# Kernel optimization log

Hardware: AMD Instinct MI355X
Metric: run time of the kernel (lower is better)

Reference implementation:

```python
import math
import jax, jax.numpy as jnp
import numpy as np

B, S, D = 4, 2048, 1024
H, HD = 16, 64
NUM_BUCKETS = 32
MAX_DISTANCE = 128
EPS = 1e-6
ENC_S = 512


def _relative_position_bucket(relative_position):
    # bidirectional=False path
    num_buckets = NUM_BUCKETS
    rp = -jnp.minimum(relative_position, 0)  # [S, S] nonneg
    max_exact = num_buckets // 2
    is_small = rp < max_exact
    scale = (num_buckets - max_exact) / math.log(MAX_DISTANCE / max_exact)
    large = max_exact + (jnp.log(jnp.maximum(rp, 1).astype(jnp.float32) / max_exact) * scale).astype(jnp.int32)
    large = jnp.minimum(large, num_buckets - 1)
    return jnp.where(is_small, rp, large)


def compute_bias(rel_emb, q_len, k_len):
    ctx = jnp.arange(q_len)[:, None]
    mem = jnp.arange(k_len)[None, :]
    bucket = _relative_position_bucket(mem - ctx)          # [q, k] int
    values = rel_emb[bucket]                                # [q, k, H]
    return jnp.transpose(values, (2, 0, 1))[None]           # [1, H, q, k]


def setup_inputs() -> dict:
    key = jax.random.key(0)
    ks = jax.random.split(key, 8)
    std = 0.02
    return {
        "input_ids": jax.random.normal(ks[0], (B, S, D), jnp.float32),
        "encoder_output": jax.random.normal(ks[1], (B, ENC_S, D), jnp.float32),
        "wq": jax.random.normal(ks[2], (D, H * HD), jnp.float32) * std,
        "wk": jax.random.normal(ks[3], (D, H * HD), jnp.float32) * std,
        "wv": jax.random.normal(ks[4], (D, H * HD), jnp.float32) * std,
        "wo": jax.random.normal(ks[5], (H * HD, D), jnp.float32) * std,
        "rel_emb": jax.random.normal(ks[6], (NUM_BUCKETS, H), jnp.float32) * std,
        "ln_w": jnp.ones((D,), jnp.float32),
    }


def reference(input_ids, encoder_output, wq, wk, wv, wo, rel_emb, ln_w):
    origin = input_ids
    # MT5LayerNorm: RMS norm, no mean subtraction, no bias
    variance = jnp.mean(jnp.square(input_ids.astype(jnp.float32)), axis=-1, keepdims=True)
    x = (input_ids * jax.lax.rsqrt(variance + EPS)) * ln_w

    q = (x @ wq).reshape(B, S, H, HD)
    k = (x @ wk).reshape(B, S, H, HD)
    v = (x @ wv).reshape(B, S, H, HD)

    # NOTE: T5-style attention has no 1/sqrt(d) scaling
    scores = jnp.einsum("bqhd,bkhd->bhqk", q, k)
    scores = scores + compute_bias(rel_emb, S, S)
    attn = jax.nn.softmax(scores, axis=-1)
    ctx = jnp.einsum("bhqk,bkhd->bqhd", attn, v).reshape(B, S, H * HD)
    attn_out = ctx @ wo

    # residual connection (dropout is identity at rate 0 / eval)
    return origin + attn_out
```

## Files before the change

### kernel.cpp

```cpp
#include <hip/hip_runtime.h>
#include <hip/hip_bf16.h>
#include <math.h>

#define S_LEN 2048
#define D_DIM 1024
#define NHEAD 16

typedef __attribute__((ext_vector_type(8))) short bf16x8;
typedef __attribute__((ext_vector_type(4))) float floatx4;

__device__ __forceinline__ short f32_bf16(float f) {
  union { float f; unsigned u; } v; v.f = f;
  unsigned r = v.u + 0x7FFFu + ((v.u >> 16) & 1u);
  return (short)(r >> 16);
}

__device__ __forceinline__ float exp2_fast(float x) {
#if __has_builtin(__builtin_amdgcn_exp2f)
  return __builtin_amdgcn_exp2f(x);
#else
  float r; asm("v_exp_f32 %0, %1" : "=v"(r) : "v"(x)); return r;
#endif
}

__device__ __forceinline__ void gload16(const void* g, void* l) {
  __builtin_amdgcn_global_load_lds((const __attribute__((address_space(1))) unsigned*)g,
                                   (__attribute__((address_space(3))) unsigned*)l,
                                   16, 0, 0);
}

__global__ __launch_bounds__(256) void prep_k(const float* __restrict__ x,
                                              const float* __restrict__ lnw,
                                              const float* __restrict__ wq,
                                              const float* __restrict__ wk,
                                              const float* __restrict__ wv,
                                              const float* __restrict__ wo,
                                              short* __restrict__ xb,
                                              short* __restrict__ oqkv,
                                              short* __restrict__ owo) {
  if (blockIdx.x < 8192) {
    int row = blockIdx.x;
    const float4* xr = (const float4*)(x + (size_t)row * D_DIM);
    float4 v = xr[threadIdx.x];
    float ss = v.x*v.x + v.y*v.y + v.z*v.z + v.w*v.w;
    #pragma unroll
    for (int off = 32; off > 0; off >>= 1) ss += __shfl_xor(ss, off);
    __shared__ float red[4];
    if ((threadIdx.x & 63) == 0) red[threadIdx.x >> 6] = ss;
    __syncthreads();
    float scale = rsqrtf((red[0]+red[1]+red[2]+red[3]) * (1.f/D_DIM) + 1e-6f);
    float4 wv4 = ((const float4*)lnw)[threadIdx.x];
    short4 o;
    o.x = f32_bf16(v.x*scale*wv4.x);
    o.y = f32_bf16(v.y*scale*wv4.y);
    o.z = f32_bf16(v.z*scale*wv4.z);
    o.w = f32_bf16(v.w*scale*wv4.w);
    ((short4*)xb)[(size_t)row*256 + threadIdx.x] = o;
  } else {
    __shared__ float tile[64][65];
    int id = blockIdx.x - 8192;
    int m  = id >> 8;
    int tt = id & 255;
    int tn = tt >> 4, tk = tt & 15;
    const float* src = (m == 0) ? wq : (m == 1) ? wk : (m == 2) ? wv : wo;
    float scale = (m == 0) ? 1.44269504f : 1.0f;
    int t = threadIdx.x;
    int kl  = t >> 4;
    int nl4 = t & 15;
    #pragma unroll
    for (int i = 0; i < 4; i++) {
      int k = i*16 + kl;
      float4 v = *(const float4*)&src[(size_t)(tk*64 + k)*1024 + tn*64 + nl4*4];
      tile[k][nl4*4+0] = v.x;
      tile[k][nl4*4+1] = v.y;
      tile[k][nl4*4+2] = v.z;
      tile[k][nl4*4+3] = v.w;
    }
    __syncthreads();
    short* dst = (m < 3) ? oqkv : owo;
    size_t nbase = (m < 3) ? (size_t)m * 1024 : 0;
    #pragma unroll
    for (int i = 0; i < 2; i++) {
      int idx = i*256 + t;
      int nl = idx >> 3;
      int g  = idx & 7;
      short tmp[8];
      #pragma unroll
      for (int j = 0; j < 8; j++) tmp[j] = f32_bf16(tile[g*8 + j][nl] * scale);
      *(bf16x8*)&dst[(nbase + tn*64 + nl)*1024 + tk*64 + g*8] = *(bf16x8*)tmp;
    }
  }
}

template<bool ADD_RES, int PANELS, bool WRITE_VT>
__global__ __launch_bounds__(256) void gemm_bt(const short* __restrict__ A,
                                               const short* __restrict__ Bt,
                                               short* __restrict__ Cb,
                                               float* __restrict__ Cf,
                                               const float* __restrict__ res,
                                               short* __restrict__ vt,
                                               int M, int N, int K) {
  constexpr int BK = 32;
  __shared__ __align__(16) short As[2][128*BK];
  __shared__ __align__(16) short Bs[2][128*BK];
  int tid = threadIdx.x;
  int w = tid >> 6, lane = tid & 63, quad = lane >> 4, l16 = lane & 15;
  int wr = w >> 1, wc = w & 1;
  const int id = blockIdx.x;
  const int xcd = id & 7, g = id >> 3;
  const int bm = g / PANELS;
  const int bn = xcd * PANELS + (g % PANELS);
  const short* Ag = A + (size_t)bm * 128 * K;
  const short* Bg = Bt + (size_t)bn * 128 * K;
  const int r4 = lane >> 2;
  const int c4 = lane & 3;
  const int lc = c4 ^ (r4 & 3);
  const int swz = (quad ^ (l16 & 3)) * 8;

  floatx4 acc[4][4] = {};

  #define GSTAGE(p_, k0_) do {                                                  \
    _Pragma("unroll")                                                           \
    for (int i = 0; i < 2; i++) {                                               \
      int c = w + i*4;                                                          \
      gload16(Ag + (size_t)(c*16 + r4) * K + (k0_) + lc*8, &As[p_][c*16*BK]);   \
      gload16(Bg + (size_t)(c*16 + r4) * K + (k0_) + lc*8, &Bs[p_][c*16*BK]);   \
    }                                                                           \
  } while (0)

  GSTAGE(0, 0);
  int p = 0;
  for (int k0 = 0; k0 < K; k0 += BK) {
    __syncthreads();
    if (k0 + BK < K) GSTAGE(p ^ 1, k0 + BK);
    bf16x8 af[4], bfr[4];
    #pragma unroll
    for (int i = 0; i < 4; i++) {
      af[i]  = *(const bf16x8*)&As[p][(wr*64 + i*16 + l16)*BK + swz];
      bfr[i] = *(const bf16x8*)&Bs[p][(wc*64 + i*16 + l16)*BK + swz];
    }
    #pragma unroll
    for (int i = 0; i < 4; i++)
      #pragma unroll
      for (int j = 0; j < 4; j++)
        acc[i][j] = __builtin_amdgcn_mfma_f32_16x16x32_bf16(af[i], bfr[j], acc[i][j], 0, 0, 0);
    p ^= 1;
  }
  #undef GSTAGE

  if (WRITE_VT && bn >= 16) {
    #pragma unroll
    for (int i = 0; i < 4; i++) {
      int row0 = bm*128 + wr*64 + i*16 + quad*4;
      int b = row0 >> 11, s = row0 & 2047;
      #pragma unroll
      for (int j = 0; j < 4; j++) {
        int hcol = bn*128 + wc*64 + j*16 + l16 - 2048;
        short4 st;
        st.x = f32_bf16(acc[i][j][0]);
        st.y = f32_bf16(acc[i][j][1]);
        st.z = f32_bf16(acc[i][j][2]);
        st.w = f32_bf16(acc[i][j][3]);
        int bh = (b << 4) + (hcol >> 6);
        *(short4*)&vt[((size_t)(bh*64 + (hcol & 63)))*2048 + s] = st;
      }
    }
    return;
  }

  #pragma unroll
  for (int i = 0; i < 4; i++) {
    int row0 = bm*128 + wr*64 + i*16 + quad*4;
    #pragma unroll
    for (int j = 0; j < 4; j++) {
      int col = bn*128 + wc*64 + j*16 + l16;
      #pragma unroll
      for (int r = 0; r < 4; r++) {
        size_t idx = (size_t)(row0 + r) * N + col;
        if (ADD_RES) Cf[idx] = res[idx] + acc[i][j][r];
        else         Cb[idx] = f32_bf16(acc[i][j][r]);
      }
    }
  }
}

__global__ __launch_bounds__(512) void flash_k(const short* __restrict__ qkv,
                                               const short* __restrict__ vt,
                                               const float* __restrict__ rel_emb,
                                               short* __restrict__ ctx) {
  __shared__ __align__(16) short Kb[2][64*64];
  __shared__ __align__(16) short Vb[2][64*64];
  __shared__ float lut2[132];

  const int L = blockIdx.x + 8*blockIdx.y;
  const int xcd = L & 7, kk_ = L >> 3;
  const int bh = xcd*8 + (kk_ >> 3);
  const int qt = kk_ & 7;
  const int b = bh >> 4, h = bh & 15;
  const int t = threadIdx.x, w = t >> 6, lane = t & 63, quad = lane >> 4, l16 = lane & 15;
  const float L2E = 1.44269504f;

  if (t < 129) {
    int rp = t, bucket;
    if (rp < 16) bucket = rp;
    else {
      bucket = 16 + (int)(logf((float)rp * 0.0625f) * (16.f / logf(8.f)));
      if (bucket > 31) bucket = 31;
    }
    lut2[t] = rel_emb[bucket*16 + h] * L2E;
  }
  const float bfut  = rel_emb[h] * L2E;
  const float bpast = rel_emb[31*16 + h] * L2E;
  const floatx4 bf4 = {bfut, bfut, bfut, bfut};
  const floatx4 bp4 = {bpast, bpast, bpast, bpast};
  const floatx4 zz4 = {0.f, 0.f, 0.f, 0.f};

  const int srow = lane >> 3;
  const int slc  = (lane & 7) ^ srow;
  const int rho  = w*8 + srow;
  const int kperm = 32*(rho >> 5) + 8*((rho >> 2) & 3) + 4*((rho >> 4) & 1) + (rho & 3);

  const short* kgU = qkv + ((size_t)b*S_LEN)*3072 + 1024 + h*64;
  const int    loK = kperm*3072 + slc*8;
  const short* vgU = vt + ((size_t)bh*64)*2048;
  const int    loV = rho*2048 + slc*8;

  bf16x8 qB[2][2];
  #pragma unroll
  for (int rb = 0; rb < 2; rb++) {
    const short* qb = qkv + ((size_t)(b*S_LEN + qt*256 + rb*128 + w*16 + l16))*3072 + h*64;
    qB[rb][0] = *(const bf16x8*)&qb[quad*8];
    qB[rb][1] = *(const bf16x8*)&qb[32 + quad*8];
  }

  floatx4 o[2][4] = {};
  floatx4 li4[2] = {};
  const short ONE = (short)0x3F80;
  bf16x8 onesA = {ONE, ONE, ONE, ONE, ONE, ONE, ONE, ONE};

  const int swz0 = (quad     ^ (l16 & 7)) * 8;
  const int swz1 = ((quad+4) ^ (l16 & 7)) * 8;

  #define STAGE(P_, KT_) do {                                                   \
    const short* ka_ = kgU + (size_t)(KT_)*196608 + loK;                        \
    gload16(ka_, &Kb[P_][(w*8)*64]);                                            \
    const short* va_ = vgU + loV + (KT_)*64;                                    \
    gload16(va_, &Vb[P_][(w*8)*64]);                                            \
  } while (0)

  #define BODY(P_, KT_) do {                                                    \
    __syncthreads();                                                            \
    if ((KT_) < 31) STAGE((P_) ^ 1, (KT_) + 1);      \
    bool boundary = ((KT_) >= 4*qt - 2) && ((KT_) <= 4*qt + 3);                 \
    floatx4 cinit = boundary ? zz4 : (((KT_) >= 4*qt) ? bf4 : bp4);             \
    floatx4 sc[2][4];                                                           \
    _Pragma("unroll")                                                           \
    for (int c = 0; c < 4; c++) {                                               \
      int rowA = (c*16 + l16)*64;                                               \
      bf16x8 ka0 = *(const bf16x8*)&Kb[P_][rowA + swz0];                        \
      bf16x8 ka1 = *(const bf16x8*)&Kb[P_][rowA + swz1];                        \
      _Pragma("unroll")                                                         \
      for (int rb = 0; rb < 2; rb++) {                                          \
        floatx4 z = __builtin_amdgcn_mfma_f32_16x16x32_bf16(ka0, qB[rb][0], cinit, 0, 0, 0); \
        z = __builtin_amdgcn_mfma_f32_16x16x32_bf16(ka1, qB[rb][1], z, 0, 0, 0);\
        sc[rb][c] = z;                                                          \
      }                                                                         \
    }                                                                           \
    if (boundary) {                                                             \
      _Pragma("unroll")                                                         \
      for (int rb = 0; rb < 2; rb++) {                                          \
        int q0 = qt*256 + rb*128 + w*16 + l16;                                  \
        _Pragma("unroll")                                                       \
        for (int c = 0; c < 4; c++) {                                           \
          int kk = (KT_)*64 + 32*(c >> 1) + 8*quad + 4*(c & 1);                 \
          _Pragma("unroll")                                                     \
          for (int r = 0; r < 4; r++) {                                         \
            int d = q0 - (kk + r);                                              \
            d = d < 0 ? 0 : (d > 128 ? 128 : d);                                \
            sc[rb][c][r] += lut2[d];                                            \
          }                                                                     \
        }                                                                       \
      }                                                                         \
    }                                                                           \
    _Pragma("unroll")                                                           \
    for (int rb = 0; rb < 2; rb++)                                              \
      _Pragma("unroll")                                                         \
      for (int c = 0; c < 4; c++)                                               \
        _Pragma("unroll")                                                       \
        for (int r = 0; r < 4; r++)                                             \
          sc[rb][c][r] = exp2_fast(sc[rb][c][r]);                               \
    bf16x8 pf[2][2];                                                            \
    _Pragma("unroll")                                                           \
    for (int rb = 0; rb < 2; rb++) {                                            \
      _Pragma("unroll")                                                         \
      for (int hh = 0; hh < 2; hh++) {                                          \
        union { bf16x8 v; unsigned u[4]; } pk;                                  \
        floatx4 a = sc[rb][2*hh], bb = sc[rb][2*hh + 1];                        \
        pk.u[0] = __builtin_amdgcn_perm(__float_as_uint(a[1]),  __float_as_uint(a[0]),  0x07060302); \
        pk.u[1] = __builtin_amdgcn_perm(__float_as_uint(a[3]),  __float_as_uint(a[2]),  0x07060302); \
        pk.u[2] = __builtin_amdgcn_perm(__float_as_uint(bb[1]), __float_as_uint(bb[0]), 0x07060302); \
        pk.u[3] = __builtin_amdgcn_perm(__float_as_uint(bb[3]), __float_as_uint(bb[2]), 0x07060302); \
        pf[rb][hh] = pk.v;                                                      \
      }                                                                         \
    }                                                                           \
    _Pragma("unroll")                                                           \
    for (int rb = 0; rb < 2; rb++) {                                            \
      li4[rb] = __builtin_amdgcn_mfma_f32_16x16x32_bf16(onesA, pf[rb][0], li4[rb], 0, 0, 0); \
      li4[rb] = __builtin_amdgcn_mfma_f32_16x16x32_bf16(onesA, pf[rb][1], li4[rb], 0, 0, 0); \
    }                                                                           \
    _Pragma("unroll")                                                           \
    for (int jj = 0; jj < 4; jj++) {                                            \
      int rowV = (jj*16 + l16)*64;                                              \
      bf16x8 va0 = *(const bf16x8*)&Vb[P_][rowV + swz0];                        \
      bf16x8 va1 = *(const bf16x8*)&Vb[P_][rowV + swz1];                        \
      _Pragma("unroll")                                                         \
      for (int rb = 0; rb < 2; rb++) {                                          \
        o[rb][jj] = __builtin_amdgcn_mfma_f32_16x16x32_bf16(va0, pf[rb][0], o[rb][jj], 0, 0, 0); \
        o[rb][jj] = __builtin_amdgcn_mfma_f32_16x16x32_bf16(va1, pf[rb][1], o[rb][jj], 0, 0, 0); \
      }                                                                         \
    }                                                                           \
  } while (0)

  STAGE(0, 0);
  for (int kt = 0; kt < 32; kt += 2) {
    BODY(0, kt);
    BODY(1, kt + 1);
  }

  #pragma unroll
  for (int rb = 0; rb < 2; rb++) {
    float inv = 1.f / li4[rb][0];
    size_t row = (size_t)(b*S_LEN + qt*256 + rb*128 + w*16 + l16);
    #pragma unroll
    for (int jj = 0; jj < 4; jj++) {
      short4 st;
      st.x = f32_bf16(o[rb][jj][0] * inv);
      st.y = f32_bf16(o[rb][jj][1] * inv);
      st.z = f32_bf16(o[rb][jj][2] * inv);
      st.w = f32_bf16(o[rb][jj][3] * inv);
      *(short4*)&ctx[row*1024 + h*64 + jj*16 + quad*4] = st;
    }
  }
  #undef STAGE
  #undef BODY
}

extern "C" void kernel_launch(void* const* d_in, const int* in_sizes, int n_in,
                              void* d_out, int out_size, void* d_ws, size_t ws_size,
                              hipStream_t stream) {
  const float* input_ids = (const float*)d_in[0];
  const float* wq      = (const float*)d_in[2];
  const float* wk      = (const float*)d_in[3];
  const float* wv      = (const float*)d_in[4];
  const float* wo      = (const float*)d_in[5];
  const float* rel_emb = (const float*)d_in[6];
  const float* ln_w    = (const float*)d_in[7];
  float* out = (float*)d_out;

  char* ws = (char*)d_ws;
  short* xb     = (short*)ws;  ws += (size_t)8192*1024*2;
  short* wqkv_t = (short*)ws;  ws += (size_t)3072*1024*2;
  short* wo_t   = (short*)ws;  ws += (size_t)1024*1024*2;
  short* qkv    = (short*)ws;  ws += (size_t)8192*3072*2;
  short* vt     = (short*)ws;  ws += (size_t)64*64*2048*2;
  short* ctx    = (short*)ws;  ws += (size_t)8192*1024*2;

  prep_k<<<8192 + 1024, 256, 0, stream>>>(input_ids, ln_w, wq, wk, wv, wo,
                                          xb, wqkv_t, wo_t);
  gemm_bt<false, 3, true><<<1536, 256, 0, stream>>>(xb, wqkv_t, qkv, nullptr,
                                                    nullptr, vt, 8192, 3072, 1024);
  flash_k<<<dim3(8, 64), 512, 0, stream>>>(qkv, vt, rel_emb, ctx);
  gemm_bt<true, 1, false><<<512, 256, 0, stream>>>(ctx, wo_t, nullptr, out,
                                                   input_ids, nullptr, 8192, 1024, 1024);
}
```

Measured before the change: 290.1 us.

## Add 256x256 four-stage pipelined GEMM for QKV projection

Replaces the 128x128 double-buffered QKV projection GEMM with a new 256x256-tile kernel using 512 threads, a 4-deep LDS ring of global-to-LDS loads, explicit waitcnt/barrier scheduling, and setprio around MFMA bursts. It also changes the LDS swizzle pattern in both GEMMs. The aim is more data reuse per tile and better overlap of memory loads with MFMA work. The trade-offs are more LDS and register pressure and only 384 blocks, which may leave some CUs underused.

```diff
diff --git a/kernel.cpp b/kernel.cpp
--- a/kernel.cpp
+++ b/kernel.cpp
@@ -92,13 +92,130 @@
   }
 }
 
-template<bool ADD_RES, int PANELS, bool WRITE_VT>
+template<bool WRITE_VT>
+__global__ __launch_bounds__(512, 2) void gemm256(const short* __restrict__ A,
+                                                  const short* __restrict__ Bt,
+                                                  short* __restrict__ Cb,
+                                                  short* __restrict__ vt,
+                                                  int N, int K, int NBN) {
+  __shared__ __align__(16) short As[4][256*32];
+  __shared__ __align__(16) short Bs[4][256*32];
+  const int tid = threadIdx.x;
+  const int w = tid >> 6, lane = tid & 63, quad = lane >> 4, l16 = lane & 15;
+  const int wm = w >> 2, wn = w & 3;
+  const int id = blockIdx.x;
+  const int o = (id & 7) * (gridDim.x >> 3) + (id >> 3);
+  const int bm = o / NBN, bn = o % NBN;
+  const short* Ag = A  + (size_t)bm * 256 * K;
+  const short* Bg = Bt + (size_t)bn * 256 * K;
+  const int r4 = lane >> 2, c4 = lane & 3;
+  const int lc  = c4 ^ ((r4 >> 1) & 3);
+  const int swz = (quad ^ ((l16 >> 1) & 3)) * 8;
+
+  floatx4 acc[8][4] = {};
+
+  #define SA(t_) do {                                                          \
+    gload16(Ag + (size_t)((w    )*16 + r4) * K + (size_t)(t_)*32 + lc*8,       \
+            &As[(t_) & 3][(w    )*512]);                                       \
+    gload16(Ag + (size_t)((w + 8)*16 + r4) * K + (size_t)(t_)*32 + lc*8,       \
+            &As[(t_) & 3][(w + 8)*512]);                                       \
+  } while (0)
+  #define SB(t_) do {                                                          \
+    gload16(Bg + (size_t)((w    )*16 + r4) * K + (size_t)(t_)*32 + lc*8,       \
+            &Bs[(t_) & 3][(w    )*512]);                                       \
+    gload16(Bg + (size_t)((w + 8)*16 + r4) * K + (size_t)(t_)*32 + lc*8,       \
+            &Bs[(t_) & 3][(w + 8)*512]);                                       \
+  } while (0)
+
+  #define PH(t_, STG_, VMW_) do {                                              \
+    const short* Ab = &As[(t_) & 3][0];                                        \
+    const short* Bb = &Bs[(t_) & 3][0];                                        \
+    bf16x8 af[8], bfr[4];                                                      \
+    _Pragma("unroll")                                                          \
+    for (int i = 0; i < 8; i++)                                                \
+      af[i] = *(const bf16x8*)&Ab[(wm*128 + i*16 + l16)*32 + swz];             \
+    bfr[0] = *(const bf16x8*)&Bb[(wn*64 +  0 + l16)*32 + swz];                 \
+    bfr[1] = *(const bf16x8*)&Bb[(wn*64 + 16 + l16)*32 + swz];                 \
+    if (STG_) SA((t_) + 3);                                                    \
+    asm volatile("s_waitcnt lgkmcnt(0)");                                      \
+    __builtin_amdgcn_sched_barrier(0);                                         \
+    __builtin_amdgcn_s_setprio(1);                                             \
+    _Pragma("unroll")                                                          \
+    for (int i = 0; i < 8; i++) {                                              \
+      acc[i][0] = __builtin_amdgcn_mfma_f32_16x16x32_bf16(af[i], bfr[0], acc[i][0], 0, 0, 0); \
+      acc[i][1] = __builtin_amdgcn_mfma_f32_16x16x32_bf16(af[i], bfr[1], acc[i][1], 0, 0, 0); \
+    }                                                                          \
+    __builtin_amdgcn_s_setprio(0);                                             \
+    bfr[2] = *(const bf16x8*)&Bb[(wn*64 + 32 + l16)*32 + swz];                 \
+    bfr[3] = *(const bf16x8*)&Bb[(wn*64 + 48 + l16)*32 + swz];                 \
+    if (STG_) SB((t_) + 3);                                                    \
+    asm volatile("s_waitcnt lgkmcnt(0)");                                      \
+    __builtin_amdgcn_sched_barrier(0);                                         \
+    __builtin_amdgcn_s_setprio(1);                                             \
+    _Pragma("unroll")                                                          \
+    for (int i = 0; i < 8; i++) {                                              \
+      acc[i][2] = __builtin_amdgcn_mfma_f32_16x16x32_bf16(af[i], bfr[2], acc[i][2], 0, 0, 0); \
+      acc[i][3] = __builtin_amdgcn_mfma_f32_16x16x32_bf16(af[i], bfr[3], acc[i][3], 0, 0, 0); \
+    }                                                                          \
+    __builtin_amdgcn_s_setprio(0);                                             \
+    asm volatile("s_waitcnt " VMW_);                                           \
+    __builtin_amdgcn_s_barrier();                                              \
+    __builtin_amdgcn_sched_barrier(0);                                         \
+  } while (0)
+
+  SA(0); SB(0); SA(1); SB(1); SA(2); SB(2);
+  asm volatile("s_waitcnt vmcnt(8)");
+  __builtin_amdgcn_s_barrier();
+  __builtin_amdgcn_sched_barrier(0);
+
+  #pragma unroll 1
+  for (int t = 0; t < 29; ++t) PH(t, true, "vmcnt(8)");
+  PH(29, false, "vmcnt(4)");
+  PH(30, false, "vmcnt(0)");
+  PH(31, false, "vmcnt(0)");
+  #undef SA
+  #undef SB
+  #undef PH
+
+  if (WRITE_VT && (bn*256 + wn*64) >= 2048) {
+    #pragma unroll
+    for (int i = 0; i < 8; i++) {
+      int row0 = bm*256 + wm*128 + i*16 + quad*4;
+      int b = row0 >> 11, s = row0 & 2047;
+      #pragma unroll
+      for (int j = 0; j < 4; j++) {
+        int hcol = bn*256 + wn*64 + j*16 + l16 - 2048;
+        short4 st;
+        st.x = f32_bf16(acc[i][j][0]);
+        st.y = f32_bf16(acc[i][j][1]);
+        st.z = f32_bf16(acc[i][j][2]);
+        st.w = f32_bf16(acc[i][j][3]);
+        int bh = (b << 4) + (hcol >> 6);
+        *(short4*)&vt[((size_t)(bh*64 + (hcol & 63)))*2048 + s] = st;
+      }
+    }
+    return;
+  }
+
+  #pragma unroll
+  for (int i = 0; i < 8; i++) {
+    int row0 = bm*256 + wm*128 + i*16 + quad*4;
+    #pragma unroll
+    for (int j = 0; j < 4; j++) {
+      int col = bn*256 + wn*64 + j*16 + l16;
+      #pragma unroll
+      for (int r = 0; r < 4; r++)
+        Cb[(size_t)(row0 + r) * N + col] = f32_bf16(acc[i][j][r]);
+    }
+  }
+}
+
+template<bool ADD_RES, int PANELS>
 __global__ __launch_bounds__(256) void gemm_bt(const short* __restrict__ A,
                                                const short* __restrict__ Bt,
                                                short* __restrict__ Cb,
                                                float* __restrict__ Cf,
                                                const float* __restrict__ res,
-                                               short* __restrict__ vt,
                                                int M, int N, int K) {
   constexpr int BK = 32;
   __shared__ __align__(16) short As[2][128*BK];
@@ -114,8 +231,8 @@
   const short* Bg = Bt + (size_t)bn * 128 * K;
   const int r4 = lane >> 2;
   const int c4 = lane & 3;
-  const int lc = c4 ^ (r4 & 3);
-  const int swz = (quad ^ (l16 & 3)) * 8;
+  const int lc = c4 ^ ((r4 >> 1) & 3);
+  const int swz = (quad ^ ((l16 >> 1) & 3)) * 8;
 
   floatx4 acc[4][4] = {};
 
@@ -147,26 +264,6 @@
     p ^= 1;
   }
   #undef GSTAGE
-
-  if (WRITE_VT && bn >= 16) {
-    #pragma unroll
-    for (int i = 0; i < 4; i++) {
-      int row0 = bm*128 + wr*64 + i*16 + quad*4;
-      int b = row0 >> 11, s = row0 & 2047;
-      #pragma unroll
-      for (int j = 0; j < 4; j++) {
-        int hcol = bn*128 + wc*64 + j*16 + l16 - 2048;
-        short4 st;
-        st.x = f32_bf16(acc[i][j][0]);
-        st.y = f32_bf16(acc[i][j][1]);
-        st.z = f32_bf16(acc[i][j][2]);
-        st.w = f32_bf16(acc[i][j][3]);
-        int bh = (b << 4) + (hcol >> 6);
-        *(short4*)&vt[((size_t)(bh*64 + (hcol & 63)))*2048 + s] = st;
-      }
-    }
-    return;
-  }
 
   #pragma unroll
   for (int i = 0; i < 4; i++) {
@@ -250,7 +347,7 @@
 
   #define BODY(P_, KT_) do {                                                    \
     __syncthreads();                                                            \
-    if ((KT_) < 31) STAGE((P_) ^ 1, (KT_) + 1);      \
+    if ((KT_) < 31) STAGE((P_) ^ 1, (KT_) + 1);                                 \
     bool boundary = ((KT_) >= 4*qt - 2) && ((KT_) <= 4*qt + 3);                 \
     floatx4 cinit = boundary ? zz4 : (((KT_) >= 4*qt) ? bf4 : bp4);             \
     floatx4 sc[2][4];                                                           \
@@ -367,9 +464,8 @@
 
   prep_k<<<8192 + 1024, 256, 0, stream>>>(input_ids, ln_w, wq, wk, wv, wo,
                                           xb, wqkv_t, wo_t);
-  gemm_bt<false, 3, true><<<1536, 256, 0, stream>>>(xb, wqkv_t, qkv, nullptr,
-                                                    nullptr, vt, 8192, 3072, 1024);
+  gemm256<true><<<384, 512, 0, stream>>>(xb, wqkv_t, qkv, vt, 3072, 1024, 12);
   flash_k<<<dim3(8, 64), 512, 0, stream>>>(qkv, vt, rel_emb, ctx);
-  gemm_bt<true, 1, false><<<512, 256, 0, stream>>>(ctx, wo_t, nullptr, out,
-                                                   input_ids, nullptr, 8192, 1024, 1024);
-}
+  gemm_bt<true, 1><<<512, 256, 0, stream>>>(ctx, wo_t, nullptr, out, input_ids,
+                                            8192, 1024, 1024);
+}
```

Result: faster. 284.0 us (-2.1%).
